# Kernel optimization log

Hardware: AMD Instinct MI355X
Metric: run time of the kernel (lower is better)

The kernel has to match this reference:

```python
import jax, jax.numpy as jnp
import numpy as np

N, D, K = 65536, 512, 4096


def setup_inputs() -> dict:
    key = jax.random.key(0)
    kx, kc = jax.random.split(key)
    x = jax.random.normal(kx, (N, D), dtype=jnp.float32)
    center = jax.random.normal(kc, (K, D), dtype=jnp.float32)
    return {"x": x, "center": center}


def squared_euclidean(x, center):
    x_sq = jnp.sum(x * x, axis=1, keepdims=True)        # [N,1]
    c_sq = jnp.sum(center * center, axis=1)             # [K]
    cross = x @ center.T                                # [N,K] GEMM
    return x_sq - 2.0 * cross + c_sq[None, :]


def reference(x, center):
    # KMeans.forward: dis_func(input, center).argmin(1)
    dist = squared_euclidean(x, center)                 # [N,K]
    return jnp.argmin(dist, axis=1)                     # [N] int32
```

## Files before the change

kernel.cpp:

```cpp
#include <hip/hip_runtime.h>

#define N_ROWS 65536
#define DIM    512
#define K_CENT 4096
#define TILE_M 128
#define TILE_N 256
#define BK     32
#define KSTEPS (DIM / BK)
#define NKT    (K_CENT / TILE_N)
#define THREADS 512
#define MARGIN 6.0f
#define CAND_CAP 3072
#define COMPACT_TRIG 2048

typedef _Float16 half8 __attribute__((ext_vector_type(8)));
typedef float floatx4 __attribute__((ext_vector_type(4)));

__device__ __forceinline__ unsigned mapF(float f) {
  unsigned u = __float_as_uint(f);
  return (u & 0x80000000u) ? ~u : (u | 0x80000000u);
}
__device__ __forceinline__ float unmapF(unsigned m) {
  unsigned u = (m & 0x80000000u) ? (m ^ 0x80000000u) : ~m;
  return __uint_as_float(u);
}

__device__ __forceinline__ void gload_lds16(const void* g, void* l) {
  __builtin_amdgcn_global_load_lds(
      (const __attribute__((address_space(1))) void*)g,
      (__attribute__((address_space(3))) void*)l, 16, 0, 0);
}

__global__ void prep_convert(const float* __restrict__ x, const float* __restrict__ c,
                             _Float16* __restrict__ xh, _Float16* __restrict__ ch,
                             float* __restrict__ csqg) {
  const size_t nx = (size_t)N_ROWS * DIM;
  const size_t nc = (size_t)K_CENT * DIM;
  size_t i = ((size_t)blockIdx.x * blockDim.x + threadIdx.x) * 8;
  if (i >= nx + nc) return;
  if (i < nx) {
    floatx4 a = *(const floatx4*)(x + i);
    floatx4 b = *(const floatx4*)(x + i + 4);
    half8 h;
#pragma unroll
    for (int e = 0; e < 4; ++e) { h[e] = (_Float16)a[e]; h[4 + e] = (_Float16)b[e]; }
    *(half8*)(xh + i) = h;
  } else {
    size_t off = i - nx;
    floatx4 a = *(const floatx4*)(c + off);
    floatx4 b = *(const floatx4*)(c + off + 4);
    half8 h;
    float s = 0.f;
#pragma unroll
    for (int e = 0; e < 4; ++e) { h[e] = (_Float16)a[e]; h[4 + e] = (_Float16)b[e]; }
#pragma unroll
    for (int e = 0; e < 8; ++e) { float v = (float)h[e]; s += v * v; }
    *(half8*)(ch + off) = h;
#pragma unroll
    for (int o = 1; o < 64; o <<= 1) s += __shfl_xor(s, o, 64);
    if ((threadIdx.x & 63) == 0) csqg[off >> 9] = s;
  }
}

template <int MODE>
__global__ __launch_bounds__(THREADS, 4)
void kmeans_argmin(const float* __restrict__ x, const float* __restrict__ cent,
                   const _Float16* __restrict__ xh, const _Float16* __restrict__ ch,
                   const float* __restrict__ csqg, int* __restrict__ out) {
  __shared__ _Float16 ldsA[TILE_M * BK];
  __shared__ _Float16 ldsB[TILE_N * BK];
  __shared__ float csq4[TILE_N][4];
  __shared__ unsigned sminU[TILE_M];
  __shared__ unsigned long long best[TILE_M];
  __shared__ unsigned candKey[CAND_CAP];
  __shared__ float candS[CAND_CAP];
  __shared__ int candCount;

  char* ldsAc = (char*)ldsA;
  char* ldsBc = (char*)ldsB;

  const int t = threadIdx.x;
  const int lane = t & 63;
  const int wave = t >> 6;
  const int wm = wave >> 2;
  const int wn = wave & 3;
  const int quad = lane >> 4;
  const int l15 = lane & 15;
  const int rowBlock = blockIdx.x * TILE_M;

  if (t < TILE_M) { sminU[t] = 0xFFFFFFFFu; best[t] = ~0ull; }
  if (t == 0) candCount = 0;

  const int srA = t >> 2;
  const int sckA = (t & 3) ^ ((srA >> 1) & 3);
  const int srB0 = t >> 2;
  const int srB1 = (t + 512) >> 2;
  const int sckB0 = (t & 3) ^ ((srB0 >> 1) & 3);
  const int sckB1 = (t & 3) ^ ((srB1 >> 1) & 3);

  for (int kt = 0; kt < NKT; ++kt) {
    const int ktBase = kt * TILE_N;
    if (MODE == 0) { ((float*)csq4)[t] = 0.f; ((float*)csq4)[t + 512] = 0.f; }
    floatx4 acc[4][4];
#pragma unroll
    for (int fm = 0; fm < 4; ++fm)
#pragma unroll
      for (int fn = 0; fn < 4; ++fn) acc[fm][fn] = (floatx4){0.f, 0.f, 0.f, 0.f};

    for (int ks = 0; ks < KSTEPS; ++ks) {
      const int kd = ks * BK;
      if (MODE == 2) {
        gload_lds16(xh + (size_t)(rowBlock + srA) * DIM + kd + sckA * 8,
                    ldsAc + (size_t)wave * 1024);
        gload_lds16(ch + (size_t)(ktBase + srB0) * DIM + kd + sckB0 * 8,
                    ldsBc + (size_t)wave * 1024);
        gload_lds16(ch + (size_t)(ktBase + srB1) * DIM + kd + sckB1 * 8,
                    ldsBc + 8192 + (size_t)wave * 1024);
      } else {
        const float* gA = x + (size_t)(rowBlock + srA) * DIM + kd + sckA * 8;
        floatx4 a0 = *(const floatx4*)gA, a1 = *(const floatx4*)(gA + 4);
        half8 ha;
#pragma unroll
        for (int e = 0; e < 4; ++e) { ha[e] = (_Float16)a0[e]; ha[4 + e] = (_Float16)a1[e]; }
        *(half8*)(ldsAc + (size_t)t * 16) = ha;
#pragma unroll
        for (int p = 0; p < 2; ++p) {
          int sr = p ? srB1 : srB0;
          int sck = p ? sckB1 : sckB0;
          int slot = p * 512 + t;
          const float* gB = cent + (size_t)(ktBase + sr) * DIM + kd + sck * 8;
          floatx4 b0 = *(const floatx4*)gB, b1 = *(const floatx4*)(gB + 4);
          half8 hb;
          float s = 0.f;
#pragma unroll
          for (int e = 0; e < 4; ++e) { hb[e] = (_Float16)b0[e]; hb[4 + e] = (_Float16)b1[e]; }
#pragma unroll
          for (int e = 0; e < 8; ++e) { float v = (float)hb[e]; s += v * v; }
          *(half8*)(ldsBc + (size_t)slot * 16) = hb;
          csq4[sr][slot & 3] += s;
        }
      }
      __syncthreads();

      half8 af[4], bf[4];
#pragma unroll
      for (int fm = 0; fm < 4; ++fm) {
        int row = wm * 64 + fm * 16 + l15;
        int slot = (row << 2) | (quad ^ ((row >> 1) & 3));
        af[fm] = *(const half8*)(ldsAc + slot * 16);
      }
#pragma unroll
      for (int fn = 0; fn < 4; ++fn) {
        int cl = wn * 64 + fn * 16 + l15;
        int slot = (cl << 2) | (quad ^ ((cl >> 1) & 3));
        bf[fn] = *(const half8*)(ldsBc + slot * 16);
      }
#pragma unroll
      for (int fm = 0; fm < 4; ++fm)
#pragma unroll
        for (int fn = 0; fn < 4; ++fn)
          acc[fm][fn] = __builtin_amdgcn_mfma_f32_16x16x32_f16(af[fm], bf[fn], acc[fm][fn], 0, 0, 0);
      __syncthreads();
    }

    float cs[4];
#pragma unroll
    for (int fn = 0; fn < 4; ++fn) {
      int cl = wn * 64 + fn * 16 + l15;
      cs[fn] = (MODE == 2) ? csqg[ktBase + cl]
                           : (csq4[cl][0] + csq4[cl][1] + csq4[cl][2] + csq4[cl][3]);
    }

#pragma unroll
    for (int fm = 0; fm < 4; ++fm)
#pragma unroll
      for (int e = 0; e < 4; ++e) {
        float v = 3.4e38f;
#pragma unroll
        for (int fn = 0; fn < 4; ++fn)
          v = fminf(v, cs[fn] - 2.f * acc[fm][fn][e]);
        v = fminf(v, __shfl_xor(v, 1, 64));
        v = fminf(v, __shfl_xor(v, 2, 64));
        v = fminf(v, __shfl_xor(v, 4, 64));
        v = fminf(v, __shfl_xor(v, 8, 64));
        if (l15 == 0)
          atomicMin(&sminU[wm * 64 + fm * 16 + quad * 4 + e], mapF(v));
      }
    __syncthreads();

    float thrR[4][4];
#pragma unroll
    for (int fm = 0; fm < 4; ++fm)
#pragma unroll
      for (int e = 0; e < 4; ++e)
        thrR[fm][e] = unmapF(sminU[wm * 64 + fm * 16 + quad * 4 + e]) + MARGIN;

#pragma unroll
    for (int fn = 0; fn < 4; ++fn) {
      int k = ktBase + wn * 64 + fn * 16 + l15;
#pragma unroll
      for (int fm = 0; fm < 4; ++fm)
#pragma unroll
        for (int e = 0; e < 4; ++e) {
          float s = cs[fn] - 2.f * acc[fm][fn][e];
          if (s <= thrR[fm][e]) {
            int idx = atomicAdd(&candCount, 1);
            if (idx < CAND_CAP) {
              candKey[idx] = ((unsigned)k << 7) | (unsigned)(wm * 64 + fm * 16 + quad * 4 + e);
              candS[idx] = s;
            }
          }
        }
    }
    __syncthreads();

    if (candCount > COMPACT_TRIG) {
      int cc = candCount; if (cc > CAND_CAP) cc = CAND_CAP;
      unsigned myK[6]; float myS[6]; int myN = 0;
      for (int i = t; i < cc; i += THREADS) {
        int rl = candKey[i] & 127;
        if (candS[i] <= unmapF(sminU[rl]) + MARGIN) {
          myK[myN] = candKey[i]; myS[myN] = candS[i]; ++myN;
        }
      }
      __syncthreads();
      if (t == 0) candCount = 0;
      __syncthreads();
      int base = atomicAdd(&candCount, myN);
      for (int j = 0; j < myN; ++j) { candKey[base + j] = myK[j]; candS[base + j] = myS[j]; }
      __syncthreads();
    }
  }

  int cnt = candCount; if (cnt > CAND_CAP) cnt = CAND_CAP;
  const int g = t >> 4;
  const int sl = t & 15;
  for (int ci = g; ci < cnt; ci += 32) {
    unsigned cd = candKey[ci];
    int rl = cd & 127;
    if (candS[ci] > unmapF(sminU[rl]) + MARGIN) continue;
    int k = cd >> 7;
    const float* xr = x + (size_t)(rowBlock + rl) * DIM;
    const float* cr = cent + (size_t)k * DIM;
    double d = 0.0;
#pragma unroll
    for (int j = 0; j < DIM / 64; ++j) {
      floatx4 xv = *(const floatx4*)(xr + j * 64 + sl * 4);
      floatx4 cv = *(const floatx4*)(cr + j * 64 + sl * 4);
#pragma unroll
      for (int e = 0; e < 4; ++e) {
        double df = (double)xv[e] - (double)cv[e];
        d += df * df;
      }
    }
#pragma unroll
    for (int off = 1; off < 16; off <<= 1) d += __shfl_xor(d, off, 64);
    if (sl == 0) {
      unsigned long long key =
          ((unsigned long long)__double_as_longlong(d) & ~0xFFFull) | (unsigned long long)k;
      atomicMin(&best[rl], key);
    }
  }
  __syncthreads();
  if (t < TILE_M) out[rowBlock + t] = (int)(best[t] & 0xFFFull);
}

extern "C" void kernel_launch(void* const* d_in, const int* in_sizes, int n_in,
                              void* d_out, int out_size, void* d_ws, size_t ws_size,
                              hipStream_t stream) {
  const float* x = (const float*)d_in[0];
  const float* cent = (const float*)d_in[1];
  int* out = (int*)d_out;
  const size_t nXh = (size_t)N_ROWS * DIM * sizeof(_Float16);
  const size_t nCh = (size_t)K_CENT * DIM * sizeof(_Float16);
  const size_t nCsq = (size_t)K_CENT * sizeof(float);
  const int grid = N_ROWS / TILE_M;

  if (ws_size >= nXh + nCh + nCsq) {
    _Float16* xh = (_Float16*)d_ws;
    _Float16* ch = (_Float16*)((char*)d_ws + nXh);
    float* csqg = (float*)((char*)d_ws + nXh + nCh);
    const size_t total8 = ((size_t)N_ROWS + K_CENT) * DIM / 8;
    prep_convert<<<(unsigned)((total8 + 255) / 256), 256, 0, stream>>>(x, cent, xh, ch, csqg);
    kmeans_argmin<2><<<grid, THREADS, 0, stream>>>(x, cent, xh, ch, csqg, out);
  } else {
    kmeans_argmin<0><<<grid, THREADS, 0, stream>>>(x, cent, nullptr, nullptr, nullptr, out);
  }
}
```

Before: 683.0 us.

## Switch distance GEMM from fp16 MFMA to fp8 scaled 32x32x64 MFMA

Quantizes x and centers to fp8 (e4m3) in the prep kernel and runs the candidate-screening GEMM with the gfx950 scaled f8f6f4 32x32x64 MFMA, doubling BK to 64 and re-laying out the LDS tiles and fragments for 32x32 outputs. The margin for candidate rescoring is widened to absorb fp8 error, while the candidate buffer is halved and the compaction step caps each thread at four survivors. The aim is to halve GEMM input bytes and raise matrix throughput. The risk is far more candidates per row under the looser margin, dropped candidates when the smaller buffer or the per-thread cap overflows, and so a wrong argmin.

Result: slower. 1.695 ms (+148.2%).

```diff
diff --git a/kernel.cpp b/kernel.cpp
--- a/kernel.cpp
+++ b/kernel.cpp
@@ -5,16 +5,20 @@
 #define K_CENT 4096
 #define TILE_M 128
 #define TILE_N 256
-#define BK     32
+#define BK     64
 #define KSTEPS (DIM / BK)
 #define NKT    (K_CENT / TILE_N)
 #define THREADS 512
-#define MARGIN 6.0f
-#define CAND_CAP 3072
-#define COMPACT_TRIG 2048
-
-typedef _Float16 half8 __attribute__((ext_vector_type(8)));
-typedef float floatx4 __attribute__((ext_vector_type(4)));
+#define MARGIN 22.0f
+#define CAND_CAP 1536
+#define COMPACT_TRIG 1024
+#define SCALE1 0x7F7F7F7F
+
+typedef float  floatx4  __attribute__((ext_vector_type(4)));
+typedef float  floatx16 __attribute__((ext_vector_type(16)));
+typedef int    intx2    __attribute__((ext_vector_type(2)));
+typedef int    intx4    __attribute__((ext_vector_type(4)));
+typedef int    intx8    __attribute__((ext_vector_type(8)));
 
 __device__ __forceinline__ unsigned mapF(float f) {
   unsigned u = __float_as_uint(f);
@@ -31,31 +35,30 @@
       (__attribute__((address_space(3))) void*)l, 16, 0, 0);
 }
 
+__device__ __forceinline__ int pk4(float a, float b, float c, float d) {
+  int r = __builtin_amdgcn_cvt_pk_fp8_f32(a, b, 0, false);
+  r = __builtin_amdgcn_cvt_pk_fp8_f32(c, d, r, true);
+  return r;
+}
+
 __global__ void prep_convert(const float* __restrict__ x, const float* __restrict__ c,
-                             _Float16* __restrict__ xh, _Float16* __restrict__ ch,
+                             unsigned char* __restrict__ xq, unsigned char* __restrict__ cq,
                              float* __restrict__ csqg) {
   const size_t nx = (size_t)N_ROWS * DIM;
-  const size_t nc = (size_t)K_CENT * DIM;
   size_t i = ((size_t)blockIdx.x * blockDim.x + threadIdx.x) * 8;
-  if (i >= nx + nc) return;
   if (i < nx) {
     floatx4 a = *(const floatx4*)(x + i);
     floatx4 b = *(const floatx4*)(x + i + 4);
-    half8 h;
-#pragma unroll
-    for (int e = 0; e < 4; ++e) { h[e] = (_Float16)a[e]; h[4 + e] = (_Float16)b[e]; }
-    *(half8*)(xh + i) = h;
-  } else {
+    intx2 q = { pk4(a[0], a[1], a[2], a[3]), pk4(b[0], b[1], b[2], b[3]) };
+    *(intx2*)(xq + i) = q;
+  } else if (i < nx + (size_t)K_CENT * DIM) {
     size_t off = i - nx;
     floatx4 a = *(const floatx4*)(c + off);
     floatx4 b = *(const floatx4*)(c + off + 4);
-    half8 h;
-    float s = 0.f;
-#pragma unroll
-    for (int e = 0; e < 4; ++e) { h[e] = (_Float16)a[e]; h[4 + e] = (_Float16)b[e]; }
-#pragma unroll
-    for (int e = 0; e < 8; ++e) { float v = (float)h[e]; s += v * v; }
-    *(half8*)(ch + off) = h;
+    intx2 q = { pk4(a[0], a[1], a[2], a[3]), pk4(b[0], b[1], b[2], b[3]) };
+    *(intx2*)(cq + off) = q;
+    float s = a[0]*a[0]+a[1]*a[1]+a[2]*a[2]+a[3]*a[3]
+            + b[0]*b[0]+b[1]*b[1]+b[2]*b[2]+b[3]*b[3];
 #pragma unroll
     for (int o = 1; o < 64; o <<= 1) s += __shfl_xor(s, o, 64);
     if ((threadIdx.x & 63) == 0) csqg[off >> 9] = s;
@@ -65,10 +68,10 @@
 template <int MODE>
 __global__ __launch_bounds__(THREADS, 4)
 void kmeans_argmin(const float* __restrict__ x, const float* __restrict__ cent,
-                   const _Float16* __restrict__ xh, const _Float16* __restrict__ ch,
+                   const unsigned char* __restrict__ xq, const unsigned char* __restrict__ cq,
                    const float* __restrict__ csqg, int* __restrict__ out) {
-  __shared__ _Float16 ldsA[TILE_M * BK];
-  __shared__ _Float16 ldsB[TILE_N * BK];
+  __shared__ unsigned char ldsA[TILE_M * BK];
+  __shared__ unsigned char ldsB[TILE_N * BK];
   __shared__ float csq4[TILE_N][4];
   __shared__ unsigned sminU[TILE_M];
   __shared__ unsigned long long best[TILE_M];
@@ -76,150 +79,159 @@
   __shared__ float candS[CAND_CAP];
   __shared__ int candCount;
 
-  char* ldsAc = (char*)ldsA;
-  char* ldsBc = (char*)ldsB;
-
   const int t = threadIdx.x;
   const int lane = t & 63;
   const int wave = t >> 6;
   const int wm = wave >> 2;
   const int wn = wave & 3;
-  const int quad = lane >> 4;
-  const int l15 = lane & 15;
+  const int l31 = lane & 31;
+  const int half = lane >> 5;
   const int rowBlock = blockIdx.x * TILE_M;
 
   if (t < TILE_M) { sminU[t] = 0xFFFFFFFFu; best[t] = ~0ull; }
   if (t == 0) candCount = 0;
 
-  const int srA = t >> 2;
-  const int sckA = (t & 3) ^ ((srA >> 1) & 3);
-  const int srB0 = t >> 2;
-  const int srB1 = (t + 512) >> 2;
-  const int sckB0 = (t & 3) ^ ((srB0 >> 1) & 3);
-  const int sckB1 = (t & 3) ^ ((srB1 >> 1) & 3);
+  const int sA = t;
+  const int rA = ((sA >> 2) & 31);
+  const int rowA = (sA >> 7) * 32 + rA;
+  const int offA = (((sA & 3) ^ ((rA >> 1) & 3)) << 4);
+  const int sB0 = t, sB1 = t + 512;
+  const int rB0 = ((sB0 >> 2) & 31);
+  const int rowB0 = (sB0 >> 7) * 32 + rB0;
+  const int offB0 = (((sB0 & 3) ^ ((rB0 >> 1) & 3)) << 4);
+  const int rB1 = ((sB1 >> 2) & 31);
+  const int rowB1 = (sB1 >> 7) * 32 + rB1;
+  const int offB1 = (((sB1 & 3) ^ ((rB1 >> 1) & 3)) << 4);
+
+  const int qk = half * 2;
+  const int fragSlotBase = 4 * l31 + (qk ^ ((l31 >> 1) & 3));
 
   for (int kt = 0; kt < NKT; ++kt) {
     const int ktBase = kt * TILE_N;
     if (MODE == 0) { ((float*)csq4)[t] = 0.f; ((float*)csq4)[t + 512] = 0.f; }
-    floatx4 acc[4][4];
-#pragma unroll
-    for (int fm = 0; fm < 4; ++fm)
-#pragma unroll
-      for (int fn = 0; fn < 4; ++fn) acc[fm][fn] = (floatx4){0.f, 0.f, 0.f, 0.f};
+    floatx16 acc[2][2];
+#pragma unroll
+    for (int fm = 0; fm < 2; ++fm)
+#pragma unroll
+      for (int fn = 0; fn < 2; ++fn)
+#pragma unroll
+        for (int e = 0; e < 16; ++e) acc[fm][fn][e] = 0.f;
 
     for (int ks = 0; ks < KSTEPS; ++ks) {
       const int kd = ks * BK;
       if (MODE == 2) {
-        gload_lds16(xh + (size_t)(rowBlock + srA) * DIM + kd + sckA * 8,
-                    ldsAc + (size_t)wave * 1024);
-        gload_lds16(ch + (size_t)(ktBase + srB0) * DIM + kd + sckB0 * 8,
-                    ldsBc + (size_t)wave * 1024);
-        gload_lds16(ch + (size_t)(ktBase + srB1) * DIM + kd + sckB1 * 8,
-                    ldsBc + 8192 + (size_t)wave * 1024);
+        gload_lds16(xq + (size_t)(rowBlock + rowA) * DIM + kd + offA,
+                    ldsA + (size_t)wave * 1024);
+        gload_lds16(cq + (size_t)(ktBase + rowB0) * DIM + kd + offB0,
+                    ldsB + (size_t)wave * 1024);
+        gload_lds16(cq + (size_t)(ktBase + rowB1) * DIM + kd + offB1,
+                    ldsB + 8192 + (size_t)wave * 1024);
       } else {
-        const float* gA = x + (size_t)(rowBlock + srA) * DIM + kd + sckA * 8;
-        floatx4 a0 = *(const floatx4*)gA, a1 = *(const floatx4*)(gA + 4);
-        half8 ha;
-#pragma unroll
-        for (int e = 0; e < 4; ++e) { ha[e] = (_Float16)a0[e]; ha[4 + e] = (_Float16)a1[e]; }
-        *(half8*)(ldsAc + (size_t)t * 16) = ha;
+        {
+          const float* gA = x + (size_t)(rowBlock + rowA) * DIM + kd + offA;
+          floatx4 f0 = *(const floatx4*)gA, f1 = *(const floatx4*)(gA + 4);
+          floatx4 f2 = *(const floatx4*)(gA + 8), f3 = *(const floatx4*)(gA + 12);
+          intx4 q = { pk4(f0[0],f0[1],f0[2],f0[3]), pk4(f1[0],f1[1],f1[2],f1[3]),
+                      pk4(f2[0],f2[1],f2[2],f2[3]), pk4(f3[0],f3[1],f3[2],f3[3]) };
+          *(intx4*)(ldsA + (size_t)sA * 16) = q;
+        }
 #pragma unroll
         for (int p = 0; p < 2; ++p) {
-          int sr = p ? srB1 : srB0;
-          int sck = p ? sckB1 : sckB0;
-          int slot = p * 512 + t;
-          const float* gB = cent + (size_t)(ktBase + sr) * DIM + kd + sck * 8;
-          floatx4 b0 = *(const floatx4*)gB, b1 = *(const floatx4*)(gB + 4);
-          half8 hb;
+          int row = p ? rowB1 : rowB0;
+          int off = p ? offB1 : offB0;
+          int slot = p ? sB1 : sB0;
+          const float* gB = cent + (size_t)(ktBase + row) * DIM + kd + off;
+          floatx4 f0 = *(const floatx4*)gB, f1 = *(const floatx4*)(gB + 4);
+          floatx4 f2 = *(const floatx4*)(gB + 8), f3 = *(const floatx4*)(gB + 12);
+          intx4 q = { pk4(f0[0],f0[1],f0[2],f0[3]), pk4(f1[0],f1[1],f1[2],f1[3]),
+                      pk4(f2[0],f2[1],f2[2],f2[3]), pk4(f3[0],f3[1],f3[2],f3[3]) };
+          *(intx4*)(ldsB + (size_t)slot * 16) = q;
           float s = 0.f;
 #pragma unroll
-          for (int e = 0; e < 4; ++e) { hb[e] = (_Float16)b0[e]; hb[4 + e] = (_Float16)b1[e]; }
-#pragma unroll
-          for (int e = 0; e < 8; ++e) { float v = (float)hb[e]; s += v * v; }
-          *(half8*)(ldsBc + (size_t)slot * 16) = hb;
-          csq4[sr][slot & 3] += s;
-        }
-      }
-      __syncthreads();
-
-      half8 af[4], bf[4];
-#pragma unroll
-      for (int fm = 0; fm < 4; ++fm) {
-        int row = wm * 64 + fm * 16 + l15;
-        int slot = (row << 2) | (quad ^ ((row >> 1) & 3));
-        af[fm] = *(const half8*)(ldsAc + slot * 16);
-      }
-#pragma unroll
-      for (int fn = 0; fn < 4; ++fn) {
-        int cl = wn * 64 + fn * 16 + l15;
-        int slot = (cl << 2) | (quad ^ ((cl >> 1) & 3));
-        bf[fn] = *(const half8*)(ldsBc + slot * 16);
-      }
-#pragma unroll
-      for (int fm = 0; fm < 4; ++fm)
-#pragma unroll
-        for (int fn = 0; fn < 4; ++fn)
-          acc[fm][fn] = __builtin_amdgcn_mfma_f32_16x16x32_f16(af[fm], bf[fn], acc[fm][fn], 0, 0, 0);
-      __syncthreads();
-    }
-
-    float cs[4];
-#pragma unroll
-    for (int fn = 0; fn < 4; ++fn) {
-      int cl = wn * 64 + fn * 16 + l15;
-      cs[fn] = (MODE == 2) ? csqg[ktBase + cl]
-                           : (csq4[cl][0] + csq4[cl][1] + csq4[cl][2] + csq4[cl][3]);
-    }
-
-#pragma unroll
-    for (int fm = 0; fm < 4; ++fm)
-#pragma unroll
-      for (int e = 0; e < 4; ++e) {
-        float v = 3.4e38f;
-#pragma unroll
-        for (int fn = 0; fn < 4; ++fn)
-          v = fminf(v, cs[fn] - 2.f * acc[fm][fn][e]);
+          for (int e = 0; e < 4; ++e)
+            s += f0[e]*f0[e] + f1[e]*f1[e] + f2[e]*f2[e] + f3[e]*f3[e];
+          csq4[row][slot & 3] += s;
+        }
+      }
+      __syncthreads();
+
+      intx8 aF[2], bF[2];
+#pragma unroll
+      for (int fm = 0; fm < 2; ++fm) {
+        int s0 = (wm * 2 + fm) * 128 + fragSlotBase;
+        intx4 lo = *(const intx4*)(ldsA + s0 * 16);
+        intx4 hi = *(const intx4*)(ldsA + (s0 ^ 1) * 16);
+        aF[fm] = (intx8){lo[0], lo[1], lo[2], lo[3], hi[0], hi[1], hi[2], hi[3]};
+      }
+#pragma unroll
+      for (int fn = 0; fn < 2; ++fn) {
+        int s0 = (wn * 2 + fn) * 128 + fragSlotBase;
+        intx4 lo = *(const intx4*)(ldsB + s0 * 16);
+        intx4 hi = *(const intx4*)(ldsB + (s0 ^ 1) * 16);
+        bF[fn] = (intx8){lo[0], lo[1], lo[2], lo[3], hi[0], hi[1], hi[2], hi[3]};
+      }
+#pragma unroll
+      for (int fm = 0; fm < 2; ++fm)
+#pragma unroll
+        for (int fn = 0; fn < 2; ++fn)
+          acc[fm][fn] = __builtin_amdgcn_mfma_scale_f32_32x32x64_f8f6f4(
+              aF[fm], bF[fn], acc[fm][fn], 0, 0, 0, SCALE1, 0, SCALE1);
+      __syncthreads();
+    }
+
+    float cs[2];
+#pragma unroll
+    for (int fn = 0; fn < 2; ++fn) {
+      int col = ktBase + wn * 64 + fn * 32 + l31;
+      cs[fn] = (MODE == 2) ? csqg[col]
+                           : (csq4[wn*64+fn*32+l31][0] + csq4[wn*64+fn*32+l31][1] +
+                              csq4[wn*64+fn*32+l31][2] + csq4[wn*64+fn*32+l31][3]);
+    }
+
+#pragma unroll
+    for (int fm = 0; fm < 2; ++fm)
+#pragma unroll
+      for (int r = 0; r < 16; ++r) {
+        float v = fminf(cs[0] - 2.f * acc[fm][0][r], cs[1] - 2.f * acc[fm][1][r]);
         v = fminf(v, __shfl_xor(v, 1, 64));
         v = fminf(v, __shfl_xor(v, 2, 64));
         v = fminf(v, __shfl_xor(v, 4, 64));
         v = fminf(v, __shfl_xor(v, 8, 64));
-        if (l15 == 0)
-          atomicMin(&sminU[wm * 64 + fm * 16 + quad * 4 + e], mapF(v));
+        v = fminf(v, __shfl_xor(v, 16, 64));
+        if (l31 == 0) {
+          int srow = wm * 64 + fm * 32 + (r & 3) + 8 * (r >> 2) + 4 * half;
+          atomicMin(&sminU[srow], mapF(v));
+        }
       }
     __syncthreads();
 
-    float thrR[4][4];
-#pragma unroll
-    for (int fm = 0; fm < 4; ++fm)
-#pragma unroll
-      for (int e = 0; e < 4; ++e)
-        thrR[fm][e] = unmapF(sminU[wm * 64 + fm * 16 + quad * 4 + e]) + MARGIN;
-
-#pragma unroll
-    for (int fn = 0; fn < 4; ++fn) {
-      int k = ktBase + wn * 64 + fn * 16 + l15;
-#pragma unroll
-      for (int fm = 0; fm < 4; ++fm)
-#pragma unroll
-        for (int e = 0; e < 4; ++e) {
-          float s = cs[fn] - 2.f * acc[fm][fn][e];
-          if (s <= thrR[fm][e]) {
+#pragma unroll
+    for (int fm = 0; fm < 2; ++fm)
+#pragma unroll
+      for (int r = 0; r < 16; ++r) {
+        int srow = wm * 64 + fm * 32 + (r & 3) + 8 * (r >> 2) + 4 * half;
+        float thr = unmapF(sminU[srow]) + MARGIN;
+#pragma unroll
+        for (int fn = 0; fn < 2; ++fn) {
+          float s = cs[fn] - 2.f * acc[fm][fn][r];
+          if (s <= thr) {
+            int k = ktBase + wn * 64 + fn * 32 + l31;
             int idx = atomicAdd(&candCount, 1);
             if (idx < CAND_CAP) {
-              candKey[idx] = ((unsigned)k << 7) | (unsigned)(wm * 64 + fm * 16 + quad * 4 + e);
+              candKey[idx] = ((unsigned)k << 7) | (unsigned)srow;
               candS[idx] = s;
             }
           }
         }
-    }
+      }
     __syncthreads();
 
     if (candCount > COMPACT_TRIG) {
       int cc = candCount; if (cc > CAND_CAP) cc = CAND_CAP;
-      unsigned myK[6]; float myS[6]; int myN = 0;
+      unsigned myK[4]; float myS[4]; int myN = 0;
       for (int i = t; i < cc; i += THREADS) {
         int rl = candKey[i] & 127;
-        if (candS[i] <= unmapF(sminU[rl]) + MARGIN) {
+        if (candS[i] <= unmapF(sminU[rl]) + MARGIN && myN < 4) {
           myK[myN] = candKey[i]; myS[myN] = candS[i]; ++myN;
         }
       }
@@ -271,18 +283,18 @@
   const float* x = (const float*)d_in[0];
   const float* cent = (const float*)d_in[1];
   int* out = (int*)d_out;
-  const size_t nXh = (size_t)N_ROWS * DIM * sizeof(_Float16);
-  const size_t nCh = (size_t)K_CENT * DIM * sizeof(_Float16);
+  const size_t nXq = (size_t)N_ROWS * DIM;
+  const size_t nCq = (size_t)K_CENT * DIM;
   const size_t nCsq = (size_t)K_CENT * sizeof(float);
   const int grid = N_ROWS / TILE_M;
 
-  if (ws_size >= nXh + nCh + nCsq) {
-    _Float16* xh = (_Float16*)d_ws;
-    _Float16* ch = (_Float16*)((char*)d_ws + nXh);
-    float* csqg = (float*)((char*)d_ws + nXh + nCh);
+  if (ws_size >= nXq + nCq + nCsq) {
+    unsigned char* xq = (unsigned char*)d_ws;
+    unsigned char* cq = xq + nXq;
+    float* csqg = (float*)(cq + nCq);
     const size_t total8 = ((size_t)N_ROWS + K_CENT) * DIM / 8;
-    prep_convert<<<(unsigned)((total8 + 255) / 256), 256, 0, stream>>>(x, cent, xh, ch, csqg);
-    kmeans_argmin<2><<<grid, THREADS, 0, stream>>>(x, cent, xh, ch, csqg, out);
+    prep_convert<<<(unsigned)((total8 + 255) / 256), 256, 0, stream>>>(x, cent, xq, cq, csqg);
+    kmeans_argmin<2><<<grid, THREADS, 0, stream>>>(x, cent, xq, cq, csqg, out);
   } else {
     kmeans_argmin<0><<<grid, THREADS, 0, stream>>>(x, cent, nullptr, nullptr, nullptr, out);
   }
```
